# Kernel optimization log

Measured on AMD Instinct MI355X. Metric: run time of the kernel, lower is better.

Reference implementation:

```python
import jax, jax.numpy as jnp
import numpy as np

N_NODES = 50000   # r_mat is [N_NODES, N_NODES] sparse
N_REL = 1000      # number of relations (rows of dual_layer)
D = 128           # node / relation feature dim
NNZ = 800000      # number of edges (nnz of r_mat)


def setup_inputs() -> dict:
    key = jax.random.key(0)
    k1, k2, k3, k4, k5, k6 = jax.random.split(key, 6)
    return {
        "inlayer": jax.random.normal(k1, (N_NODES, D), jnp.float32),
        "dual_layer": jax.random.normal(k2, (N_REL, D), jnp.float32),
        # Conv1d(in=D, out=1, kernel=1): weight [1, D, 1] -> vector [D], bias [1]
        "conv_w": jax.random.normal(k3, (D,), jnp.float32) * (1.0 / np.sqrt(D)),
        "conv_b": jax.random.normal(k4, (1,), jnp.float32) * 0.01,
        # COO indices of r_mat: row = destination node, col = source node
        "edge_idx": jax.random.randint(k5, (2, NNZ), 0, N_NODES, dtype=jnp.int32),
        # r_mat._values(): integer relation id per edge
        "edge_rel": jax.random.randint(k6, (NNZ,), 0, N_REL, dtype=jnp.int32),
    }


def reference(inlayer, dual_layer, conv_w, conv_b, edge_idx, edge_rel):
    # conv1d with kernel_size=1 over [1, D, n_rel] == per-relation linear -> [n_rel]
    scores = dual_layer @ conv_w + conv_b[0]
    # gather per-edge logit by relation id
    logits = scores[edge_rel]                                  # [nnz]
    # NOTE: original applies leaky_relu then softmax GLOBALLY over all nnz edges
    coefs = jax.nn.softmax(jax.nn.leaky_relu(logits))          # [nnz]
    row, col = edge_idx[0], edge_idx[1]
    # sparse-dense matmul: out[r] = sum_{e: row[e]=r} coefs[e] * inlayer[col[e]]
    out = jax.ops.segment_sum(coefs[:, None] * inlayer[col], row,
                              num_segments=N_NODES)            # [N, D]
    # act_func=None path of the original forward
    return out
```

## Files before the change

### kernel.cpp

```cpp
#include <hip/hip_runtime.h>
#include <hip/hip_fp16.h>
#include <math.h>

#define N_NODES 50000
#define N_REL   1000
#define D       128
#define NNZ     800000

#define RB    128
#define NBIN  391
#define CAP   2560
#define CH    2048
#define NCH   ((NNZ + CH - 1) / CH)
#define K1T   512
#define K1E   (CH / K1T)
#define PBT   512
#define PE    (CAP / PBT)

__global__ void __launch_bounds__(K1T)
k1_kernel(const int* __restrict__ rows, const int* __restrict__ cols,
          const int* __restrict__ rel, const float* __restrict__ dual,
          const float* __restrict__ conv_w, const float* __restrict__ conv_b,
          const float* __restrict__ inlayer, float* __restrict__ exp_scores,
          unsigned* __restrict__ bincur, unsigned long long* __restrict__ binbuf,
          __half2* __restrict__ hinl) {
    __shared__ unsigned long long sbuf[CH];
    __shared__ unsigned short sbin[CH];
    __shared__ unsigned lcnt[NBIN], lstart[NBIN], lgb[NBIN];
    __shared__ unsigned wsum[8];
    int t = threadIdx.x;
    int gtid = blockIdx.x * K1T + t;
    int lane = t & 63, w = t >> 6;

    int wid = gtid >> 6;
    if (wid < N_REL) {
        const float* row = dual + (long)wid * D;
        float s = row[lane] * conv_w[lane] + row[lane + 64] * conv_w[lane + 64];
        #pragma unroll
        for (int off = 32; off > 0; off >>= 1) s += __shfl_down(s, off);
        if (lane == 0) {
            float v = s + conv_b[0];
            v = (v >= 0.f) ? v : 0.01f * v;
            exp_scores[wid] = expf(v);
        }
    }

    const float4* src4 = (const float4*)inlayer;
    uint2* dst2 = (uint2*)hinl;
    for (int i = gtid; i < N_NODES * D / 4; i += NCH * K1T) {
        float4 f = src4[i];
        __half2 h0 = __floats2half2_rn(f.x, f.y);
        __half2 h1 = __floats2half2_rn(f.z, f.w);
        uint2 o; o.x = *(unsigned*)&h0; o.y = *(unsigned*)&h1;
        dst2[i] = o;
    }

    for (int i = t; i < NBIN; i += K1T) lcnt[i] = 0;
    __syncthreads();

    int base = blockIdx.x * CH;
    int n = NNZ - base; if (n > CH) n = CH;
    int base4 = blockIdx.x * (CH / 4);

    int       ebin[K1E];
    unsigned  erank[K1E];
    unsigned long long epack[K1E];
    bool has = (4 * t < n);
    int4 rr, cc, qq;
    if (has) {
        rr = ((const int4*)rows)[base4 + t];
        cc = ((const int4*)cols)[base4 + t];
        qq = ((const int4*)rel)[base4 + t];
    }
    #pragma unroll
    for (int k = 0; k < K1E; ++k) {
        if (has) {
            int r = (k == 0) ? rr.x : (k == 1) ? rr.y : (k == 2) ? rr.z : rr.w;
            int c = (k == 0) ? cc.x : (k == 1) ? cc.y : (k == 2) ? cc.z : cc.w;
            int q = (k == 0) ? qq.x : (k == 1) ? qq.y : (k == 2) ? qq.z : qq.w;
            int b = r >> 7;
            epack[k] = (unsigned long long)(unsigned)c
                     | ((unsigned long long)(unsigned)q << 16)
                     | ((unsigned long long)(unsigned)(r & 127) << 26);
            ebin[k] = b;
            erank[k] = atomicAdd(&lcnt[b], 1u);
        } else ebin[k] = -1;
    }
    __syncthreads();

    unsigned cb = (t < NBIN) ? lcnt[t] : 0u;
    unsigned v = cb;
    #pragma unroll
    for (int off = 1; off < 64; off <<= 1) {
        unsigned y = __shfl_up(v, off);
        if (lane >= off) v += y;
    }
    if (lane == 63) wsum[w] = v;
    __syncthreads();
    if (t == 0) {
        unsigned acc = 0;
        #pragma unroll
        for (int k = 0; k < 8; ++k) { unsigned tmp = wsum[k]; wsum[k] = acc; acc += tmp; }
    }
    __syncthreads();
    if (t < NBIN) {
        lstart[t] = wsum[w] + (v - cb);
        lgb[t] = atomicAdd(&bincur[t * 16], cb);
    }
    __syncthreads();

    #pragma unroll
    for (int k = 0; k < K1E; ++k) {
        if (ebin[k] >= 0) {
            unsigned p = lstart[ebin[k]] + erank[k];
            sbuf[p] = epack[k];
            sbin[p] = (unsigned short)ebin[k];
        }
    }
    __syncthreads();

    #pragma unroll
    for (int k = 0; k < K1E; ++k) {
        int j = k * K1T + t;
        if (j < n) {
            int b = sbin[j];
            unsigned slot = lgb[b] + (unsigned)j - lstart[b];
            if (slot < CAP)
                binbuf[(unsigned long long)b * CAP + slot] = sbuf[j];
        }
    }
}

__global__ void __launch_bounds__(PBT)
place_kernel(const unsigned* __restrict__ bincur,
             const unsigned long long* __restrict__ binbuf,
             const float* __restrict__ exp_scores,
             unsigned* __restrict__ starts, unsigned* __restrict__ bpack,
             float* __restrict__ denom) {
    __shared__ unsigned cnt[RB], cur[RB], ex[RB];
    __shared__ unsigned wsum[8];
    __shared__ float    rpart[8];
    __shared__ unsigned sh_binbase;
    int t = threadIdx.x, lane = t & 63, w = t >> 6;
    int b = blockIdx.x;
    int rlo = b * RB;
    unsigned nb = bincur[b * 16]; if (nb > CAP) nb = CAP;
    const unsigned long long* bb = binbuf + (unsigned long long)b * CAP;

    if (t < RB) { cnt[t] = 0; cur[t] = 0; }
    __syncthreads();

    unsigned long long epk[PE];
    #pragma unroll
    for (int k = 0; k < PE; ++k) {
        int e = t + k * PBT;
        if (e < (int)nb) {
            unsigned long long pk = bb[e];
            epk[k] = pk;
            atomicAdd(&cnt[(pk >> 26) & 127ULL], 1u);
        }
    }

    unsigned bv = (t < b) ? min(bincur[t * 16], (unsigned)CAP) : 0u;
    #pragma unroll
    for (int off = 32; off > 0; off >>= 1) bv += __shfl_down(bv, off);
    if (lane == 0) wsum[w] = bv;
    __syncthreads();
    if (t == 0) {
        unsigned s = 0;
        #pragma unroll
        for (int k = 0; k < 8; ++k) s += wsum[k];
        sh_binbase = s;
    }
    __syncthreads();

    unsigned c0 = (t < RB) ? cnt[t] : 0u;
    unsigned v = c0;
    #pragma unroll
    for (int off = 1; off < 64; off <<= 1) {
        unsigned y = __shfl_up(v, off);
        if (lane >= off) v += y;
    }
    if (lane == 63) wsum[w] = v;
    __syncthreads();
    if (t == 0) {
        unsigned acc = 0;
        #pragma unroll
        for (int k = 0; k < 8; ++k) { unsigned tmp = wsum[k]; wsum[k] = acc; acc += tmp; }
    }
    __syncthreads();
    unsigned gex = sh_binbase + wsum[w] + (v - c0);
    if (t < RB) ex[t] = gex;
    if (t <= RB && rlo + t <= N_NODES)
        starts[rlo + t] = gex;
    __syncthreads();

    float dsum = 0.f;
    #pragma unroll
    for (int k = 0; k < PE; ++k) {
        int e = t + k * PBT;
        if (e < (int)nb) {
            unsigned long long pk = epk[k];
            int r = (int)((pk >> 26) & 127ULL);
            unsigned lp = (unsigned)(pk & 0x3FFFFFFULL);
            unsigned rank = atomicAdd(&cur[r], 1u);
            bpack[ex[r] + rank] = lp;
            dsum += exp_scores[lp >> 16];
        }
    }
    #pragma unroll
    for (int off = 32; off > 0; off >>= 1) dsum += __shfl_down(dsum, off);
    if (lane == 0) rpart[w] = dsum;
    __syncthreads();
    if (t == 0) {
        float s = 0.f;
        #pragma unroll
        for (int k = 0; k < 8; ++k) s += rpart[k];
        atomicAdd(denom, s);
    }
}

__global__ void gather_kernel(const unsigned* __restrict__ starts,
                              const unsigned* __restrict__ bpack,
                              const float* __restrict__ exp_scores,
                              const __half2* __restrict__ hinl,
                              const float* __restrict__ denom,
                              float* __restrict__ out) {
    int node = blockIdx.x * (blockDim.x >> 6) + (threadIdx.x >> 6);
    int lane = threadIdx.x & 63;
    if (node >= N_NODES) return;
    int s = (int)starts[node];
    int e = (int)starts[node + 1];
    int quad = lane >> 4;
    int l16  = lane & 15;
    float a0=0.f,a1=0.f,a2=0.f,a3=0.f,a4=0.f,a5=0.f,a6=0.f,a7=0.f;
    for (int base = s; base < e; base += 64) {
        int rem = e - base; if (rem > 64) rem = 64;
        int px = 0, py = 0;
        if (lane < rem) {
            unsigned pk = bpack[base + lane];
            px = (int)(pk & 0xFFFFu);
            py = __float_as_int(exp_scores[pk >> 16]);
        }
        for (int j = 0; j < rem; j += 16) {
            #pragma unroll
            for (int k = 0; k < 16; k += 4) {
                if (j + k < rem) {
                    int idx = j + k + quad;
                    int   c = __shfl(px, idx);
                    float wv = __int_as_float(__shfl(py, idx));
                    const __half2* hp = hinl + (long)c * (D / 2) + l16 * 4;
                    uint4 hv = *(const uint4*)hp;
                    float2 f0 = __half22float2(*(const __half2*)&hv.x);
                    float2 f1 = __half22float2(*(const __half2*)&hv.y);
                    float2 f2 = __half22float2(*(const __half2*)&hv.z);
                    float2 f3 = __half22float2(*(const __half2*)&hv.w);
                    a0 += wv * f0.x; a1 += wv * f0.y;
                    a2 += wv * f1.x; a3 += wv * f1.y;
                    a4 += wv * f2.x; a5 += wv * f2.y;
                    a6 += wv * f3.x; a7 += wv * f3.y;
                }
            }
        }
    }
    #define COMB(x) x += __shfl(x, lane ^ 16); x += __shfl(x, lane ^ 32);
    COMB(a0) COMB(a1) COMB(a2) COMB(a3) COMB(a4) COMB(a5) COMB(a6) COMB(a7)
    #undef COMB
    if (lane < 32) {
        float inv = 1.0f / *denom;
        float4 v;
        int hi = (lane >> 4) & 1;
        if (hi) { v.x = a4*inv; v.y = a5*inv; v.z = a6*inv; v.w = a7*inv; }
        else    { v.x = a0*inv; v.y = a1*inv; v.z = a2*inv; v.w = a3*inv; }
        *(float4*)(out + (long)node * D + l16 * 8 + hi * 4) = v;
    }
}

extern "C" void kernel_launch(void* const* d_in, const int* in_sizes, int n_in,
                              void* d_out, int out_size, void* d_ws, size_t ws_size,
                              hipStream_t stream) {
    const float* inlayer  = (const float*)d_in[0];
    const float* dual     = (const float*)d_in[1];
    const float* conv_w   = (const float*)d_in[2];
    const float* conv_b   = (const float*)d_in[3];
    const int*   edge_idx = (const int*)d_in[4];
    const int*   edge_rel = (const int*)d_in[5];
    float* out = (float*)d_out;
    const int* rows = edge_idx;
    const int* cols = edge_idx + NNZ;

    char* ws = (char*)d_ws;
    float*              exp_scores = (float*)             (ws);
    float*              denom      = (float*)             (ws + 4096);
    unsigned*           bincur     = (unsigned*)          (ws + 8192);
    unsigned*           starts     = (unsigned*)          (ws + 36864);
    unsigned long long* binbuf     = (unsigned long long*)(ws + 245760);
    unsigned*           bpack      = (unsigned*)          (ws + 245760 + 8007680);
    __half2*            hinl       = (__half2*)           (ws + 245760 + 8007680 + 3200000);

    hipMemsetAsync(ws + 4096, 0, 4096 + NBIN * 64, stream);

    k1_kernel<<<NCH, K1T, 0, stream>>>(rows, cols, edge_rel, dual, conv_w, conv_b,
                                       inlayer, exp_scores, bincur, binbuf, hinl);
    place_kernel<<<NBIN, PBT, 0, stream>>>(bincur, binbuf, exp_scores,
                                           starts, bpack, denom);
    int grid = (N_NODES + 3) / 4;
    gather_kernel<<<grid, 256, 0, stream>>>(starts, bpack, exp_scores,
                                            hinl, denom, out);
}
```

Measured before the change: 143.3 us.

## Replace block-local binning with direct global atomics and 32-bit packed bins

The edge binning kernel drops its shared-memory local sort and prefix scan and instead appends each edge to its bin with a per-edge global atomic, using a grid-stride loop over a fixed grid. Bins are halved to 64 rows so the packed edge fits in 32 bits, halving bin buffer traffic and simplifying the place kernel's scan to a single wave. The trade is many contended global atomics and uncoalesced scattered writes in place of block-aggregated ones.

```diff
diff --git a/kernel.cpp b/kernel.cpp
--- a/kernel.cpp
+++ b/kernel.cpp
@@ -7,30 +7,24 @@
 #define D       128
 #define NNZ     800000
 
-#define RB    128
-#define NBIN  391
-#define CAP   2560
-#define CH    2048
-#define NCH   ((NNZ + CH - 1) / CH)
+#define RB    64
+#define NBIN  782
+#define CAP   1280
+#define NBK1  768
 #define K1T   512
-#define K1E   (CH / K1T)
 #define PBT   512
-#define PE    (CAP / PBT)
+#define PE    3
 
 __global__ void __launch_bounds__(K1T)
 k1_kernel(const int* __restrict__ rows, const int* __restrict__ cols,
           const int* __restrict__ rel, const float* __restrict__ dual,
           const float* __restrict__ conv_w, const float* __restrict__ conv_b,
           const float* __restrict__ inlayer, float* __restrict__ exp_scores,
-          unsigned* __restrict__ bincur, unsigned long long* __restrict__ binbuf,
+          unsigned* __restrict__ bincur, unsigned* __restrict__ binbuf,
           __half2* __restrict__ hinl) {
-    __shared__ unsigned long long sbuf[CH];
-    __shared__ unsigned short sbin[CH];
-    __shared__ unsigned lcnt[NBIN], lstart[NBIN], lgb[NBIN];
-    __shared__ unsigned wsum[8];
     int t = threadIdx.x;
     int gtid = blockIdx.x * K1T + t;
-    int lane = t & 63, w = t >> 6;
+    int lane = t & 63;
 
     int wid = gtid >> 6;
     if (wid < N_REL) {
@@ -47,7 +41,7 @@
 
     const float4* src4 = (const float4*)inlayer;
     uint2* dst2 = (uint2*)hinl;
-    for (int i = gtid; i < N_NODES * D / 4; i += NCH * K1T) {
+    for (int i = gtid; i < N_NODES * D / 4; i += NBK1 * K1T) {
         float4 f = src4[i];
         __half2 h0 = __floats2half2_rn(f.x, f.y);
         __half2 h1 = __floats2half2_rn(f.z, f.w);
@@ -55,85 +49,29 @@
         dst2[i] = o;
     }
 
-    for (int i = t; i < NBIN; i += K1T) lcnt[i] = 0;
-    __syncthreads();
-
-    int base = blockIdx.x * CH;
-    int n = NNZ - base; if (n > CH) n = CH;
-    int base4 = blockIdx.x * (CH / 4);
-
-    int       ebin[K1E];
-    unsigned  erank[K1E];
-    unsigned long long epack[K1E];
-    bool has = (4 * t < n);
-    int4 rr, cc, qq;
-    if (has) {
-        rr = ((const int4*)rows)[base4 + t];
-        cc = ((const int4*)cols)[base4 + t];
-        qq = ((const int4*)rel)[base4 + t];
-    }
-    #pragma unroll
-    for (int k = 0; k < K1E; ++k) {
-        if (has) {
+    const int4* r4 = (const int4*)rows;
+    const int4* c4 = (const int4*)cols;
+    const int4* q4 = (const int4*)rel;
+    for (int j = gtid; j < NNZ / 4; j += NBK1 * K1T) {
+        int4 rr = r4[j]; int4 cc = c4[j]; int4 qq = q4[j];
+        #pragma unroll
+        for (int k = 0; k < 4; ++k) {
             int r = (k == 0) ? rr.x : (k == 1) ? rr.y : (k == 2) ? rr.z : rr.w;
             int c = (k == 0) ? cc.x : (k == 1) ? cc.y : (k == 2) ? cc.z : cc.w;
             int q = (k == 0) ? qq.x : (k == 1) ? qq.y : (k == 2) ? qq.z : qq.w;
-            int b = r >> 7;
-            epack[k] = (unsigned long long)(unsigned)c
-                     | ((unsigned long long)(unsigned)q << 16)
-                     | ((unsigned long long)(unsigned)(r & 127) << 26);
-            ebin[k] = b;
-            erank[k] = atomicAdd(&lcnt[b], 1u);
-        } else ebin[k] = -1;
-    }
-    __syncthreads();
-
-    unsigned cb = (t < NBIN) ? lcnt[t] : 0u;
-    unsigned v = cb;
-    #pragma unroll
-    for (int off = 1; off < 64; off <<= 1) {
-        unsigned y = __shfl_up(v, off);
-        if (lane >= off) v += y;
-    }
-    if (lane == 63) wsum[w] = v;
-    __syncthreads();
-    if (t == 0) {
-        unsigned acc = 0;
-        #pragma unroll
-        for (int k = 0; k < 8; ++k) { unsigned tmp = wsum[k]; wsum[k] = acc; acc += tmp; }
-    }
-    __syncthreads();
-    if (t < NBIN) {
-        lstart[t] = wsum[w] + (v - cb);
-        lgb[t] = atomicAdd(&bincur[t * 16], cb);
-    }
-    __syncthreads();
-
-    #pragma unroll
-    for (int k = 0; k < K1E; ++k) {
-        if (ebin[k] >= 0) {
-            unsigned p = lstart[ebin[k]] + erank[k];
-            sbuf[p] = epack[k];
-            sbin[p] = (unsigned short)ebin[k];
-        }
-    }
-    __syncthreads();
-
-    #pragma unroll
-    for (int k = 0; k < K1E; ++k) {
-        int j = k * K1T + t;
-        if (j < n) {
-            int b = sbin[j];
-            unsigned slot = lgb[b] + (unsigned)j - lstart[b];
-            if (slot < CAP)
-                binbuf[(unsigned long long)b * CAP + slot] = sbuf[j];
+            int b = r >> 6;
+            unsigned pk = (unsigned)c | ((unsigned)q << 16)
+                        | ((unsigned)(r & 63) << 26);
+            unsigned pos = atomicAdd(&bincur[b * 16], 1u);
+            if (pos < CAP)
+                binbuf[(unsigned)b * CAP + pos] = pk;
         }
     }
 }
 
 __global__ void __launch_bounds__(PBT)
 place_kernel(const unsigned* __restrict__ bincur,
-             const unsigned long long* __restrict__ binbuf,
+             const unsigned* __restrict__ binbuf,
              const float* __restrict__ exp_scores,
              unsigned* __restrict__ starts, unsigned* __restrict__ bpack,
              float* __restrict__ denom) {
@@ -145,23 +83,24 @@
     int b = blockIdx.x;
     int rlo = b * RB;
     unsigned nb = bincur[b * 16]; if (nb > CAP) nb = CAP;
-    const unsigned long long* bb = binbuf + (unsigned long long)b * CAP;
+    const unsigned* bb = binbuf + (unsigned)b * CAP;
 
     if (t < RB) { cnt[t] = 0; cur[t] = 0; }
     __syncthreads();
 
-    unsigned long long epk[PE];
+    unsigned epk[PE];
     #pragma unroll
     for (int k = 0; k < PE; ++k) {
         int e = t + k * PBT;
         if (e < (int)nb) {
-            unsigned long long pk = bb[e];
+            unsigned pk = bb[e];
             epk[k] = pk;
-            atomicAdd(&cnt[(pk >> 26) & 127ULL], 1u);
-        }
-    }
-
-    unsigned bv = (t < b) ? min(bincur[t * 16], (unsigned)CAP) : 0u;
+            atomicAdd(&cnt[pk >> 26], 1u);
+        }
+    }
+
+    unsigned bv = 0;
+    for (int i = t; i < b; i += PBT) bv += min(bincur[i * 16], (unsigned)CAP);
     #pragma unroll
     for (int off = 32; off > 0; off >>= 1) bv += __shfl_down(bv, off);
     if (lane == 0) wsum[w] = bv;
@@ -172,40 +111,32 @@
         for (int k = 0; k < 8; ++k) s += wsum[k];
         sh_binbase = s;
     }
-    __syncthreads();
-
-    unsigned c0 = (t < RB) ? cnt[t] : 0u;
-    unsigned v = c0;
-    #pragma unroll
-    for (int off = 1; off < 64; off <<= 1) {
-        unsigned y = __shfl_up(v, off);
-        if (lane >= off) v += y;
-    }
-    if (lane == 63) wsum[w] = v;
-    __syncthreads();
-    if (t == 0) {
-        unsigned acc = 0;
-        #pragma unroll
-        for (int k = 0; k < 8; ++k) { unsigned tmp = wsum[k]; wsum[k] = acc; acc += tmp; }
-    }
-    __syncthreads();
-    unsigned gex = sh_binbase + wsum[w] + (v - c0);
-    if (t < RB) ex[t] = gex;
-    if (t <= RB && rlo + t <= N_NODES)
-        starts[rlo + t] = gex;
-    __syncthreads();
+
+    if (t < 64) {
+        unsigned c0 = cnt[t];
+        unsigned v = c0;
+        #pragma unroll
+        for (int off = 1; off < 64; off <<= 1) {
+            unsigned y = __shfl_up(v, off);
+            if (lane >= off) v += y;
+        }
+        ex[t] = v - c0;
+    }
+    __syncthreads();
+    unsigned base = sh_binbase;
+    if (t < RB && rlo + t <= N_NODES)
+        starts[rlo + t] = base + ex[t];
 
     float dsum = 0.f;
     #pragma unroll
     for (int k = 0; k < PE; ++k) {
         int e = t + k * PBT;
         if (e < (int)nb) {
-            unsigned long long pk = epk[k];
-            int r = (int)((pk >> 26) & 127ULL);
-            unsigned lp = (unsigned)(pk & 0x3FFFFFFULL);
+            unsigned pk = epk[k];
+            int r = (int)(pk >> 26);
             unsigned rank = atomicAdd(&cur[r], 1u);
-            bpack[ex[r] + rank] = lp;
-            dsum += exp_scores[lp >> 16];
+            bpack[base + ex[r] + rank] = pk & 0x3FFFFFFu;
+            dsum += exp_scores[(pk >> 16) & 0x3FFu];
         }
     }
     #pragma unroll
@@ -290,18 +221,18 @@
     const int* cols = edge_idx + NNZ;
 
     char* ws = (char*)d_ws;
-    float*              exp_scores = (float*)             (ws);
-    float*              denom      = (float*)             (ws + 4096);
-    unsigned*           bincur     = (unsigned*)          (ws + 8192);
-    unsigned*           starts     = (unsigned*)          (ws + 36864);
-    unsigned long long* binbuf     = (unsigned long long*)(ws + 245760);
-    unsigned*           bpack      = (unsigned*)          (ws + 245760 + 8007680);
-    __half2*            hinl       = (__half2*)           (ws + 245760 + 8007680 + 3200000);
+    float*    exp_scores = (float*)   (ws);
+    float*    denom      = (float*)   (ws + 4096);
+    unsigned* bincur     = (unsigned*)(ws + 8192);
+    unsigned* starts     = (unsigned*)(ws + 65536);
+    unsigned* binbuf     = (unsigned*)(ws + 266240);
+    unsigned* bpack      = (unsigned*)(ws + 4270080);
+    __half2*  hinl       = (__half2*) (ws + 7470080);
 
     hipMemsetAsync(ws + 4096, 0, 4096 + NBIN * 64, stream);
 
-    k1_kernel<<<NCH, K1T, 0, stream>>>(rows, cols, edge_rel, dual, conv_w, conv_b,
-                                       inlayer, exp_scores, bincur, binbuf, hinl);
+    k1_kernel<<<NBK1, K1T, 0, stream>>>(rows, cols, edge_rel, dual, conv_w, conv_b,
+                                        inlayer, exp_scores, bincur, binbuf, hinl);
     place_kernel<<<NBIN, PBT, 0, stream>>>(bincur, binbuf, exp_scores,
                                            starts, bpack, denom);
     int grid = (N_NODES + 3) / 4;
```

Result: slower. 176.4 us (+23.1%).
